# Performance work log

Measured on AMD Instinct MI355X. Metric: run time of the kernel, lower is better.

Reference implementation:

```python
import jax, jax.numpy as jnp
import numpy as np

NUM_CLASSES = 80
D_IMG = 2048
D_WORD = 300
D_MID = 1024
B = 8
CONV = 14


def setup_inputs() -> dict:
    key = jax.random.key(0)
    ks = jax.random.split(key, 6)
    s = lambda k, shape, sc: jax.random.normal(k, shape, dtype=jnp.float32) * sc
    return {
        "batch_size": B,
        "img_feature_map": jax.random.normal(ks[0], (B, D_IMG, CONV, CONV), dtype=jnp.float32),
        "word_features": jax.random.normal(ks[1], (NUM_CLASSES, D_WORD), dtype=jnp.float32),
        "W1": s(ks[2], (D_MID, D_IMG), 0.02),
        "W2": s(ks[3], (D_MID, D_WORD), 0.02),
        "W3": s(ks[4], (D_MID, D_MID), 0.02),
        "b3": jnp.zeros((D_MID,), jnp.float32),
        "Wa": s(ks[5], (1, D_MID), 0.02),
        "ba": jnp.zeros((1,), jnp.float32),
    }


def reference(batch_size, img_feature_map, word_features, W1, W2, W3, b3, Wa, ba):
    # img_feature_map: [B, D_img, H, W] -> [B, H, W, D_img] (matches torch double transpose)
    Bn, D, H, W = img_feature_map.shape
    fmap = jnp.transpose(img_feature_map, (0, 2, 3, 1))                 # [B,H,W,D]
    f_wh = jnp.einsum('bhwd,md->bhwm', fmap, W1)                        # fc_1: [B,H,W,M]
    f_wd = word_features @ W2.T                                         # fc_2: [C,M]
    # broadcast multiply (no explicit repeat) + tanh
    t = jnp.tanh(f_wh[:, :, :, None, :] * f_wd)                         # [B,H,W,C,M]
    lb = jnp.einsum('bhwcm,nm->bhwcn', t, W3) + b3                      # fc_3: [B,H,W,C,M]
    coef = jnp.einsum('bhwcm,m->bhwc', lb, Wa[0]) + ba[0]               # fc_a: [B,H,W,C]
    # softmax over spatial positions per (batch, class)
    C = coef.shape[-1]
    coef = jax.nn.softmax(coef.reshape(Bn, H * W, C), axis=1).reshape(Bn, H, W, C)
    # softmax-weighted spatial pooling -> [B, C, D]
    return jnp.einsum('bhwc,bhwd->bcd', coef, fmap)
```

## Files before the change

### kernel.cpp

```cpp
#include <hip/hip_runtime.h>
#include <hip/hip_bf16.h>
#include <stdint.h>

#define NB 8
#define DIMG 2048
#define HWN 196
#define PN 1568
#define DMID 1024
#define NC 80
#define DWORD 300
#define PART 8

typedef short bf16x8 __attribute__((ext_vector_type(8)));
typedef float f32x4 __attribute__((ext_vector_type(4)));

__device__ __forceinline__ unsigned short f2bf(float x) {
  union { float f; unsigned u; } c; c.f = x;
  unsigned r = c.u + 0x7FFFu + ((c.u >> 16) & 1u);
  return (unsigned short)(r >> 16);
}

__global__ void k_tc(const float* __restrict__ img, unsigned short* __restrict__ fmapH,
                     const float* __restrict__ W1, unsigned short* __restrict__ W1h) {
  __shared__ float tile[32][33];
  int bx = blockIdx.x;
  int tx = threadIdx.x, ty = threadIdx.y;
  if (bx < 3584) {
    int d0 = (bx & 63) * 32;
    int rem = bx >> 6;
    int h0 = (rem % 7) * 32, b = rem / 7;
    const float* src = img + (size_t)b * DIMG * HWN;
#pragma unroll
    for (int i = 0; i < 32; i += 8) {
      int hw = h0 + tx;
      tile[ty + i][tx] = (hw < HWN) ? src[(size_t)(d0 + ty + i) * HWN + hw] : 0.f;
    }
    __syncthreads();
#pragma unroll
    for (int i = 0; i < 32; i += 8) {
      int hw = h0 + ty + i;
      if (hw < HWN)
        fmapH[(size_t)(b * HWN + hw) * DIMG + d0 + tx] = f2bf(tile[tx][ty + i]);
    }
  } else {
    int tid = ty * 32 + tx;
    int i = ((bx - 3584) * 256 + tid) * 4;
    f32x4 v = *(const f32x4*)(W1 + i);
    ushort4 s;
    s.x = f2bf(v[0]); s.y = f2bf(v[1]); s.z = f2bf(v[2]); s.w = f2bf(v[3]);
    *(ushort4*)(W1h + i) = s;
  }
}

__global__ __launch_bounds__(256) void k_fwdweff(const float* __restrict__ word,
                                                 const float* __restrict__ W2,
                                                 float* __restrict__ fwd,
                                                 const float* __restrict__ Wa,
                                                 const float* __restrict__ W3,
                                                 float* __restrict__ partial) {
  __shared__ __align__(16) float w2s[64 * DWORD];
  __shared__ __align__(16) float wds[16 * DWORD];
  int bx = blockIdx.x, t = threadIdx.x;
  if (bx < 80) {
    int m0 = (bx & 15) * 64, c0 = (bx >> 4) * 16;
    const float SC = 2.8853900817779268f;
    for (int u = t; u < 64 * 75; u += 256) {
      int r = u / 75, q = u - r * 75;
      *(f32x4*)&w2s[r * DWORD + q * 4] =
          *(const f32x4*)(W2 + (size_t)(m0 + r) * DWORD + q * 4);
    }
    for (int u = t; u < 16 * 75; u += 256) {
      int r = u / 75, q = u - r * 75;
      f32x4 v = *(const f32x4*)(word + (size_t)(c0 + r) * DWORD + q * 4);
      *(f32x4*)&wds[r * DWORD + q * 4] = v * SC;
    }
    __syncthreads();
    int ci = t >> 4, mi = t & 15;
    f32x4 a0 = {0.f, 0.f, 0.f, 0.f}, a1 = a0, a2 = a0, a3 = a0;
    const float* wr = &wds[ci * DWORD];
    for (int q = 0; q < 75; ++q) {
      f32x4 wv = *(const f32x4*)&wr[q * 4];
      f32x4 b0 = *(const f32x4*)&w2s[(mi)*DWORD + q * 4];
      f32x4 b1 = *(const f32x4*)&w2s[(mi + 16) * DWORD + q * 4];
      f32x4 b2 = *(const f32x4*)&w2s[(mi + 32) * DWORD + q * 4];
      f32x4 b3 = *(const f32x4*)&w2s[(mi + 48) * DWORD + q * 4];
#pragma unroll
      for (int u = 0; u < 4; ++u) {
        a0[u] = fmaf(wv[u], b0[u], a0[u]);
        a1[u] = fmaf(wv[u], b1[u], a1[u]);
        a2[u] = fmaf(wv[u], b2[u], a2[u]);
        a3[u] = fmaf(wv[u], b3[u], a3[u]);
      }
    }
    float* dst = fwd + (size_t)(c0 + ci) * DMID + m0 + mi;
    dst[0]  = a0[0] + a0[1] + a0[2] + a0[3];
    dst[16] = a1[0] + a1[1] + a1[2] + a1[3];
    dst[32] = a2[0] + a2[1] + a2[2] + a2[3];
    dst[48] = a3[0] + a3[1] + a3[2] + a3[3];
  } else {
    int idx = bx - 80;
    int m = (idx & 3) * 256 + t;
    int n0 = (idx >> 2) * 64;
    float acc = 0.f;
    for (int n = n0; n < n0 + 64; ++n) acc = fmaf(Wa[n], W3[(size_t)n * DMID + m], acc);
    partial[(size_t)(idx >> 2) * DMID + m] = acc;
  }
}

#define GLDS(g, l) \
  __builtin_amdgcn_global_load_lds((const __attribute__((address_space(1))) void*)(g), \
                                   (__attribute__((address_space(3))) void*)(l), 16, 0, 0)

__global__ __launch_bounds__(256) void k_gemm(const unsigned short* __restrict__ A,
                                              const unsigned short* __restrict__ Bw,
                                              float* __restrict__ C) {
  __shared__ __align__(16) unsigned short As[3][64 * 64];
  __shared__ __align__(16) unsigned short Bs[3][64 * 64];
  int m0 = blockIdx.x * 64, n0 = blockIdx.y * 64;
  int t = threadIdx.x;
  int w = t >> 6, l = t & 63;
  int wr = w >> 1, wc = w & 1;
  f32x4 zero = {0.f, 0.f, 0.f, 0.f};
  f32x4 acc00 = zero, acc01 = zero, acc10 = zero, acc11 = zero;

  int r0 = t >> 3, c0 = t & 7;
  int r1 = r0 + 32;
  const unsigned short* ga0 = A + (size_t)(m0 + r0) * 2048 + ((c0 ^ (r0 & 7)) << 3);
  const unsigned short* ga1 = A + (size_t)(m0 + r1) * 2048 + ((c0 ^ (r1 & 7)) << 3);
  const unsigned short* gb0 = Bw + (size_t)(n0 + r0) * 2048 + ((c0 ^ (r0 & 7)) << 3);
  const unsigned short* gb1 = Bw + (size_t)(n0 + r1) * 2048 + ((c0 ^ (r1 & 7)) << 3);

  int ra = wr * 32 + (l & 15);
  int rb = wc * 32 + (l & 15);
  int cc = l >> 4;
  int a_k0 = ra * 64 + (((cc) ^ (ra & 7)) << 3);
  int a_k1 = ra * 64 + (((cc + 4) ^ (ra & 7)) << 3);
  int b_k0 = rb * 64 + (((cc) ^ (rb & 7)) << 3);
  int b_k1 = rb * 64 + (((cc + 4) ^ (rb & 7)) << 3);

#define STAGE(bi, kk) do { \
    GLDS(ga0 + (kk), &As[bi][t * 8]); \
    GLDS(ga1 + (kk), &As[bi][t * 8 + 2048]); \
    GLDS(gb0 + (kk), &Bs[bi][t * 8]); \
    GLDS(gb1 + (kk), &Bs[bi][t * 8 + 2048]); \
  } while (0)

#define COMPUTE(bi) do { \
    const unsigned short* ap = As[bi]; \
    const unsigned short* bp = Bs[bi]; \
    bf16x8 A0 = *(const bf16x8*)(ap + a_k0); \
    bf16x8 A1 = *(const bf16x8*)(ap + a_k0 + 1024); \
    bf16x8 B0 = *(const bf16x8*)(bp + b_k0); \
    bf16x8 B1 = *(const bf16x8*)(bp + b_k0 + 1024); \
    acc00 = __builtin_amdgcn_mfma_f32_16x16x32_bf16(A0, B0, acc00, 0, 0, 0); \
    acc01 = __builtin_amdgcn_mfma_f32_16x16x32_bf16(A0, B1, acc01, 0, 0, 0); \
    acc10 = __builtin_amdgcn_mfma_f32_16x16x32_bf16(A1, B0, acc10, 0, 0, 0); \
    acc11 = __builtin_amdgcn_mfma_f32_16x16x32_bf16(A1, B1, acc11, 0, 0, 0); \
    bf16x8 A2 = *(const bf16x8*)(ap + a_k1); \
    bf16x8 A3 = *(const bf16x8*)(ap + a_k1 + 1024); \
    bf16x8 B2 = *(const bf16x8*)(bp + b_k1); \
    bf16x8 B3 = *(const bf16x8*)(bp + b_k1 + 1024); \
    acc00 = __builtin_amdgcn_mfma_f32_16x16x32_bf16(A2, B2, acc00, 0, 0, 0); \
    acc01 = __builtin_amdgcn_mfma_f32_16x16x32_bf16(A2, B3, acc01, 0, 0, 0); \
    acc10 = __builtin_amdgcn_mfma_f32_16x16x32_bf16(A3, B2, acc10, 0, 0, 0); \
    acc11 = __builtin_amdgcn_mfma_f32_16x16x32_bf16(A3, B3, acc11, 0, 0, 0); \
  } while (0)

  STAGE(0, 0);
  STAGE(1, 64);
  asm volatile("s_waitcnt vmcnt(4)" ::: "memory");
  __builtin_amdgcn_s_barrier();
  __builtin_amdgcn_sched_barrier(0);
  for (int kt = 0; kt < 32; ++kt) {
    int cur = kt % 3;
    if (kt < 30) STAGE((kt + 2) % 3, (kt + 2) * 64);
    COMPUTE(cur);
    if (kt < 30) {
      asm volatile("s_waitcnt vmcnt(4)" ::: "memory");
      __builtin_amdgcn_s_barrier();
      __builtin_amdgcn_sched_barrier(0);
    } else if (kt == 30) {
      asm volatile("s_waitcnt vmcnt(0)" ::: "memory");
      __builtin_amdgcn_s_barrier();
      __builtin_amdgcn_sched_barrier(0);
    }
  }
  int cr = (l >> 4) << 2, ccn = l & 15;
#pragma unroll
  for (int q = 0; q < 4; ++q) {
    C[(size_t)(m0 + wr * 32 + cr + q) * DMID + n0 + wc * 32 + ccn] = acc00[q];
    C[(size_t)(m0 + wr * 32 + cr + q) * DMID + n0 + wc * 32 + 16 + ccn] = acc01[q];
    C[(size_t)(m0 + wr * 32 + 16 + cr + q) * DMID + n0 + wc * 32 + ccn] = acc10[q];
    C[(size_t)(m0 + wr * 32 + 16 + cr + q) * DMID + n0 + wc * 32 + 16 + ccn] = acc11[q];
  }
#undef STAGE
#undef COMPUTE
}

#define MC 128
__global__ __launch_bounds__(256) void k_coef(const float* __restrict__ fwh,
                                              const float* __restrict__ fwd,
                                              const float* __restrict__ partial,
                                              float* __restrict__ coefp) {
  __shared__ __align__(16) float al[64][132];
  __shared__ __align__(16) float bl[16][132];
  __shared__ __align__(16) float wl[MC];
  int p0 = blockIdx.x * 64, c0 = blockIdx.y * 16, mz = blockIdx.z;
  int mbase = mz * MC;
  int t = threadIdx.x;
  {
    int sra = t >> 2, sca = (t & 3) << 5;
    const float* gA = fwh + (size_t)(p0 + sra) * DMID + mbase + sca;
#pragma unroll
    for (int q = 0; q < 8; ++q)
      *(f32x4*)&al[sra][sca + q * 4] = *(const f32x4*)&gA[q * 4];
    int srb = t >> 4, scb = (t & 15) << 3;
    const float* gB = fwd + (size_t)(c0 + srb) * DMID + mbase + scb;
#pragma unroll
    for (int q = 0; q < 2; ++q)
      *(f32x4*)&bl[srb][scb + q * 4] = *(const f32x4*)&gB[q * 4];
    if (t < MC) {
      float v = 0.f;
#pragma unroll
      for (int s = 0; s < 16; ++s) v += partial[(size_t)s * DMID + mbase + t];
      wl[t] = -2.f * v;
    }
  }
  __syncthreads();
  int pi = t >> 4, ci = t & 15;
  float acc[4];
#pragma unroll
  for (int j = 0; j < 4; ++j) acc[j] = 0.f;

  for (int mm = 0; mm < MC; mm += 4) {
    f32x4 wv = *(const f32x4*)&wl[mm];
    f32x4 bv = *(const f32x4*)&bl[ci][mm];
    f32x4 av0 = *(const f32x4*)&al[pi][mm];
    f32x4 av1 = *(const f32x4*)&al[pi + 16][mm];
    f32x4 av2 = *(const f32x4*)&al[pi + 32][mm];
    f32x4 av3 = *(const f32x4*)&al[pi + 48][mm];
#pragma unroll
    for (int u = 0; u < 4; ++u) {
      float w = wv[u], b = bv[u];
      float e0 = __builtin_amdgcn_exp2f(av0[u] * b);
      float e1 = __builtin_amdgcn_exp2f(av1[u] * b);
      float e2 = __builtin_amdgcn_exp2f(av2[u] * b);
      float e3 = __builtin_amdgcn_exp2f(av3[u] * b);
      acc[0] = fmaf(w, __builtin_amdgcn_rcpf(1.f + e0), acc[0]);
      acc[1] = fmaf(w, __builtin_amdgcn_rcpf(1.f + e1), acc[1]);
      acc[2] = fmaf(w, __builtin_amdgcn_rcpf(1.f + e2), acc[2]);
      acc[3] = fmaf(w, __builtin_amdgcn_rcpf(1.f + e3), acc[3]);
    }
  }
  float* cp = coefp + (size_t)mz * (PN * NC);
#pragma unroll
  for (int j = 0; j < 4; ++j) {
    int p = p0 + pi + 16 * j;
    if (p < PN) cp[(size_t)p * NC + c0 + ci] = acc[j];
  }
}

__global__ __launch_bounds__(256) void k_pool(const float* __restrict__ coefp,
                                              const float* __restrict__ img,
                                              float* __restrict__ out) {
  __shared__ __align__(16) float wt[HWN][16];
  __shared__ float red[16][16];
  __shared__ float mxs[16], inv[16];
  int dc = blockIdx.x * 256, cg = blockIdx.y * 16, b = blockIdx.z;
  int t = threadIdx.x;
  for (int i = t; i < HWN * 4; i += 256) {
    int hw = i >> 2, j4 = (i & 3) << 2;
    size_t o = (size_t)(b * HWN + hw) * NC + cg + j4;
    f32x4 s = {0.f, 0.f, 0.f, 0.f};
#pragma unroll
    for (int z = 0; z < PART; ++z) s += *(const f32x4*)&coefp[o + (size_t)z * (PN * NC)];
    *(f32x4*)&wt[hw][j4] = s;
  }
  __syncthreads();
  int j = t & 15, g = t >> 4;
  float pm = -1e30f;
  for (int hw = g; hw < HWN; hw += 16) pm = fmaxf(pm, wt[hw][j]);
  red[g][j] = pm;
  __syncthreads();
  if (t < 16) {
    float m = red[0][t];
#pragma unroll
    for (int g2 = 1; g2 < 16; ++g2) m = fmaxf(m, red[g2][t]);
    mxs[t] = m;
  }
  __syncthreads();
  float mj = mxs[j], ps = 0.f;
  for (int hw = g; hw < HWN; hw += 16) {
    float e = __builtin_amdgcn_exp2f((wt[hw][j] - mj) * 1.4426950408889634f);
    wt[hw][j] = e;
    ps += e;
  }
  red[g][j] = ps;
  __syncthreads();
  if (t < 16) {
    float s = 0.f;
#pragma unroll
    for (int g2 = 0; g2 < 16; ++g2) s += red[g2][t];
    inv[t] = 1.f / s;
  }
  __syncthreads();
  float acc[16];
#pragma unroll
  for (int q = 0; q < 16; ++q) acc[q] = 0.f;
  const float* fpd = img + ((size_t)b * DIMG + dc + t) * HWN;
  for (int hw = 0; hw < HWN; ++hw) {
    float v = fpd[hw];
#pragma unroll
    for (int q = 0; q < 16; ++q) acc[q] = fmaf(wt[hw][q], v, acc[q]);
  }
#pragma unroll
  for (int q = 0; q < 16; ++q)
    out[((size_t)b * NC + cg + q) * DIMG + dc + t] = acc[q] * inv[q];
}

extern "C" void kernel_launch(void* const* d_in, const int* in_sizes, int n_in,
                              void* d_out, int out_size, void* d_ws, size_t ws_size,
                              hipStream_t stream) {
  const float* img  = (const float*)d_in[1];
  const float* word = (const float*)d_in[2];
  const float* W1   = (const float*)d_in[3];
  const float* W2   = (const float*)d_in[4];
  const float* W3   = (const float*)d_in[5];
  const float* Wa   = (const float*)d_in[7];
  float* out = (float*)d_out;
  char* ws = (char*)d_ws;

  unsigned short* fmapH   = (unsigned short*)(ws + 0);
  unsigned short* W1h     = (unsigned short*)(ws + 6553600);
  float*          fwh     = (float*)(ws + 10747904);
  float*          fwd     = (float*)(ws + 17301504);
  float*          partial = (float*)(ws + 17694720);
  float*          coefp   = (float*)(ws + 17760256);

  hipLaunchKernelGGL(k_tc, dim3(5632), dim3(32, 8), 0, stream, img, fmapH, W1, W1h);
  hipLaunchKernelGGL(k_fwdweff, dim3(144), dim3(256), 0, stream,
                     word, W2, fwd, Wa, W3, partial);
  hipLaunchKernelGGL(k_gemm, dim3(25, 16), dim3(256), 0, stream, fmapH, W1h, fwh);
  hipLaunchKernelGGL(k_coef, dim3(25, 5, 8), dim3(256), 0, stream, fwh, fwd, partial, coefp);
  hipLaunchKernelGGL(k_pool, dim3(8, 5, 8), dim3(256), 0, stream, coefp, img, out);
  (void)in_sizes; (void)n_in; (void)out_size; (void)ws_size;
}
```

Before: 114.1 us.

## Split GEMM K dimension in two and sum partials in coef kernel

```diff
diff --git a/kernel.cpp b/kernel.cpp
--- a/kernel.cpp
+++ b/kernel.cpp
@@ -117,6 +117,7 @@
   __shared__ __align__(16) unsigned short As[3][64 * 64];
   __shared__ __align__(16) unsigned short Bs[3][64 * 64];
   int m0 = blockIdx.x * 64, n0 = blockIdx.y * 64;
+  int koff = blockIdx.z * 1024;
   int t = threadIdx.x;
   int w = t >> 6, l = t & 63;
   int wr = w >> 1, wc = w & 1;
@@ -125,10 +126,10 @@
 
   int r0 = t >> 3, c0 = t & 7;
   int r1 = r0 + 32;
-  const unsigned short* ga0 = A + (size_t)(m0 + r0) * 2048 + ((c0 ^ (r0 & 7)) << 3);
-  const unsigned short* ga1 = A + (size_t)(m0 + r1) * 2048 + ((c0 ^ (r1 & 7)) << 3);
-  const unsigned short* gb0 = Bw + (size_t)(n0 + r0) * 2048 + ((c0 ^ (r0 & 7)) << 3);
-  const unsigned short* gb1 = Bw + (size_t)(n0 + r1) * 2048 + ((c0 ^ (r1 & 7)) << 3);
+  const unsigned short* ga0 = A + (size_t)(m0 + r0) * 2048 + koff + ((c0 ^ (r0 & 7)) << 3);
+  const unsigned short* ga1 = A + (size_t)(m0 + r1) * 2048 + koff + ((c0 ^ (r1 & 7)) << 3);
+  const unsigned short* gb0 = Bw + (size_t)(n0 + r0) * 2048 + koff + ((c0 ^ (r0 & 7)) << 3);
+  const unsigned short* gb1 = Bw + (size_t)(n0 + r1) * 2048 + koff + ((c0 ^ (r1 & 7)) << 3);
 
   int ra = wr * 32 + (l & 15);
   int rb = wc * 32 + (l & 15);
@@ -171,85 +172,93 @@
   asm volatile("s_waitcnt vmcnt(4)" ::: "memory");
   __builtin_amdgcn_s_barrier();
   __builtin_amdgcn_sched_barrier(0);
-  for (int kt = 0; kt < 32; ++kt) {
+  for (int kt = 0; kt < 16; ++kt) {
     int cur = kt % 3;
-    if (kt < 30) STAGE((kt + 2) % 3, (kt + 2) * 64);
+    if (kt < 14) STAGE((kt + 2) % 3, (kt + 2) * 64);
     COMPUTE(cur);
-    if (kt < 30) {
+    if (kt < 14) {
       asm volatile("s_waitcnt vmcnt(4)" ::: "memory");
       __builtin_amdgcn_s_barrier();
       __builtin_amdgcn_sched_barrier(0);
-    } else if (kt == 30) {
+    } else if (kt == 14) {
       asm volatile("s_waitcnt vmcnt(0)" ::: "memory");
       __builtin_amdgcn_s_barrier();
       __builtin_amdgcn_sched_barrier(0);
     }
   }
+  float* Cz = C + (size_t)blockIdx.z * (1600 * DMID);
   int cr = (l >> 4) << 2, ccn = l & 15;
 #pragma unroll
   for (int q = 0; q < 4; ++q) {
-    C[(size_t)(m0 + wr * 32 + cr + q) * DMID + n0 + wc * 32 + ccn] = acc00[q];
-    C[(size_t)(m0 + wr * 32 + cr + q) * DMID + n0 + wc * 32 + 16 + ccn] = acc01[q];
-    C[(size_t)(m0 + wr * 32 + 16 + cr + q) * DMID + n0 + wc * 32 + ccn] = acc10[q];
-    C[(size_t)(m0 + wr * 32 + 16 + cr + q) * DMID + n0 + wc * 32 + 16 + ccn] = acc11[q];
+    Cz[(size_t)(m0 + wr * 32 + cr + q) * DMID + n0 + wc * 32 + ccn] = acc00[q];
+    Cz[(size_t)(m0 + wr * 32 + cr + q) * DMID + n0 + wc * 32 + 16 + ccn] = acc01[q];
+    Cz[(size_t)(m0 + wr * 32 + 16 + cr + q) * DMID + n0 + wc * 32 + ccn] = acc10[q];
+    Cz[(size_t)(m0 + wr * 32 + 16 + cr + q) * DMID + n0 + wc * 32 + 16 + ccn] = acc11[q];
   }
 #undef STAGE
 #undef COMPUTE
 }
 
-#define MC 128
-__global__ __launch_bounds__(256) void k_coef(const float* __restrict__ fwh,
+#define MC 64
+__global__ __launch_bounds__(256) void k_coef(const float* __restrict__ fwhp,
                                               const float* __restrict__ fwd,
                                               const float* __restrict__ partial,
                                               float* __restrict__ coefp) {
-  __shared__ __align__(16) float al[64][132];
-  __shared__ __align__(16) float bl[16][132];
+  __shared__ __align__(16) float al[64][68];
+  __shared__ __align__(16) float bl[16][68];
   __shared__ __align__(16) float wl[MC];
   int p0 = blockIdx.x * 64, c0 = blockIdx.y * 16, mz = blockIdx.z;
-  int mbase = mz * MC;
   int t = threadIdx.x;
-  {
-    int sra = t >> 2, sca = (t & 3) << 5;
-    const float* gA = fwh + (size_t)(p0 + sra) * DMID + mbase + sca;
-#pragma unroll
-    for (int q = 0; q < 8; ++q)
-      *(f32x4*)&al[sra][sca + q * 4] = *(const f32x4*)&gA[q * 4];
-    int srb = t >> 4, scb = (t & 15) << 3;
-    const float* gB = fwd + (size_t)(c0 + srb) * DMID + mbase + scb;
-#pragma unroll
-    for (int q = 0; q < 2; ++q)
-      *(f32x4*)&bl[srb][scb + q * 4] = *(const f32x4*)&gB[q * 4];
-    if (t < MC) {
-      float v = 0.f;
-#pragma unroll
-      for (int s = 0; s < 16; ++s) v += partial[(size_t)s * DMID + mbase + t];
-      wl[t] = -2.f * v;
-    }
-  }
-  __syncthreads();
   int pi = t >> 4, ci = t & 15;
   float acc[4];
 #pragma unroll
   for (int j = 0; j < 4; ++j) acc[j] = 0.f;
 
-  for (int mm = 0; mm < MC; mm += 4) {
-    f32x4 wv = *(const f32x4*)&wl[mm];
-    f32x4 bv = *(const f32x4*)&bl[ci][mm];
-    f32x4 av0 = *(const f32x4*)&al[pi][mm];
-    f32x4 av1 = *(const f32x4*)&al[pi + 16][mm];
-    f32x4 av2 = *(const f32x4*)&al[pi + 32][mm];
-    f32x4 av3 = *(const f32x4*)&al[pi + 48][mm];
-#pragma unroll
-    for (int u = 0; u < 4; ++u) {
-      float w = wv[u], b = bv[u];
-      float e0 = __builtin_amdgcn_exp2f(av0[u] * b);
-      float e1 = __builtin_amdgcn_exp2f(av1[u] * b);
-      float e2 = __builtin_amdgcn_exp2f(av2[u] * b);
-      float e3 = __builtin_amdgcn_exp2f(av3[u] * b);
-      acc[0] = fmaf(w, __builtin_amdgcn_rcpf(1.f + e0), acc[0]);
-      acc[1] = fmaf(w, __builtin_amdgcn_rcpf(1.f + e1), acc[1]);
-      acc[2] = fmaf(w, __builtin_amdgcn_rcpf(1.f + e2), acc[2]);
-      acc[3] = fmaf(w, __builtin_amdgcn_rcpf(1.f + e3), acc[3]);
+  const float* fwh0 = fwhp;
+  const float* fwh1 = fwhp + (size_t)1600 * DMID;
+
+  for (int mc = 0; mc < 2; ++mc) {
+    int mbase = mz * 128 + mc * MC;
+    __syncthreads();
+    {
+      int sra = t >> 2, sca = (t & 3) << 4;
+      const float* gA0 = fwh0 + (size_t)(p0 + sra) * DMID + mbase + sca;
+      const float* gA1 = fwh1 + (size_t)(p0 + sra) * DMID + mbase + sca;
+#pragma unroll
+      for (int q = 0; q < 4; ++q) {
+        f32x4 v = *(const f32x4*)&gA0[q * 4];
+        f32x4 u = *(const f32x4*)&gA1[q * 4];
+        *(f32x4*)&al[sra][sca + q * 4] = v + u;
+      }
+      int srb = t >> 4, scb = (t & 15) << 2;
+      *(f32x4*)&bl[srb][scb] = *(const f32x4*)(fwd + (size_t)(c0 + srb) * DMID + mbase + scb);
+      if (t < MC) {
+        float v = 0.f;
+#pragma unroll
+        for (int s = 0; s < 16; ++s) v += partial[(size_t)s * DMID + mbase + t];
+        wl[t] = -2.f * v;
+      }
+    }
+    __syncthreads();
+    for (int mm = 0; mm < MC; mm += 4) {
+      f32x4 wv = *(const f32x4*)&wl[mm];
+      f32x4 bv = *(const f32x4*)&bl[ci][mm];
+      f32x4 av0 = *(const f32x4*)&al[pi][mm];
+      f32x4 av1 = *(const f32x4*)&al[pi + 16][mm];
+      f32x4 av2 = *(const f32x4*)&al[pi + 32][mm];
+      f32x4 av3 = *(const f32x4*)&al[pi + 48][mm];
+#pragma unroll
+      for (int u = 0; u < 4; ++u) {
+        float w = wv[u], b = bv[u];
+        float e0 = __builtin_amdgcn_exp2f(av0[u] * b);
+        float e1 = __builtin_amdgcn_exp2f(av1[u] * b);
+        float e2 = __builtin_amdgcn_exp2f(av2[u] * b);
+        float e3 = __builtin_amdgcn_exp2f(av3[u] * b);
+        acc[0] = fmaf(w, __builtin_amdgcn_rcpf(1.f + e0), acc[0]);
+        acc[1] = fmaf(w, __builtin_amdgcn_rcpf(1.f + e1), acc[1]);
+        acc[2] = fmaf(w, __builtin_amdgcn_rcpf(1.f + e2), acc[2]);
+        acc[3] = fmaf(w, __builtin_amdgcn_rcpf(1.f + e3), acc[3]);
+      }
     }
   }
   float* cp = coefp + (size_t)mz * (PN * NC);
@@ -332,16 +341,16 @@
 
   unsigned short* fmapH   = (unsigned short*)(ws + 0);
   unsigned short* W1h     = (unsigned short*)(ws + 6553600);
-  float*          fwh     = (float*)(ws + 10747904);
-  float*          fwd     = (float*)(ws + 17301504);
-  float*          partial = (float*)(ws + 17694720);
-  float*          coefp   = (float*)(ws + 17760256);
+  float*          fwhp    = (float*)(ws + 10747904);
+  float*          fwd     = (float*)(ws + 23855104);
+  float*          partial = (float*)(ws + 24248320);
+  float*          coefp   = (float*)(ws + 24313856);
 
   hipLaunchKernelGGL(k_tc, dim3(5632), dim3(32, 8), 0, stream, img, fmapH, W1, W1h);
   hipLaunchKernelGGL(k_fwdweff, dim3(144), dim3(256), 0, stream,
                      word, W2, fwd, Wa, W3, partial);
-  hipLaunchKernelGGL(k_gemm, dim3(25, 16), dim3(256), 0, stream, fmapH, W1h, fwh);
-  hipLaunchKernelGGL(k_coef, dim3(25, 5, 8), dim3(256), 0, stream, fwh, fwd, partial, coefp);
+  hipLaunchKernelGGL(k_gemm, dim3(25, 16, 2), dim3(256), 0, stream, fmapH, W1h, fwhp);
+  hipLaunchKernelGGL(k_coef, dim3(25, 5, 8), dim3(256), 0, stream, fwhp, fwd, partial, coefp);
   hipLaunchKernelGGL(k_pool, dim3(8, 5, 8), dim3(256), 0, stream, coefp, img, out);
   (void)in_sizes; (void)n_in; (void)out_size; (void)ws_size;
 }
```

Result: no change. 113.3 us (-0.7%).
